# Kernel tuning notes

Measured on AMD Instinct MI355X. Metric: run time of the kernel, lower is better.

Reference implementation:

```python
import jax, jax.numpy as jnp
import numpy as np

MAX_H = 22
NUM_HEADS = 8
EPS = 1e-5
SLOPE = 0.01  # torch LeakyReLU default


def setup_inputs() -> dict:
    key = jax.random.key(0)
    ks = jax.random.split(key, 8)
    n, c, s, h, w = 16, 64, 30, 64, 22
    cp, v = 64, 17
    p, out_c = 7, 256
    D = c * MAX_H + cp * 2  # fuse_dim = 1536
    sil = jax.random.normal(ks[0], (n, c, s, h, w), dtype=jnp.float32)
    pose = jax.random.normal(ks[1], (n, cp, s, v), dtype=jnp.float32)
    min_idx = jax.random.randint(ks[2], (p, n), 0, h - MAX_H + 1, dtype=jnp.int32)
    max_idx = min_idx + MAX_H  # slices are exactly MAX_H rows (static shape)
    fc_bin = jax.random.normal(ks[3], (p, D, out_c), dtype=jnp.float32) * np.sqrt(2.0 / (D + out_c))
    gamma = 1.0 + 0.1 * jax.random.normal(ks[4], (out_c,), dtype=jnp.float32)
    beta = 0.1 * jax.random.normal(ks[5], (out_c,), dtype=jnp.float32)
    w_qkv = jax.random.normal(ks[6], (3 * out_c, out_c), dtype=jnp.float32) * 0.02
    w_proj = jax.random.normal(ks[7], (out_c, out_c), dtype=jnp.float32) * 0.02
    return {"sil": sil, "pose": pose, "fc_bin": fc_bin, "gamma": gamma, "beta": beta,
            "w_qkv": w_qkv, "w_proj": w_proj, "min_idx": min_idx, "max_idx": max_idx}


def _forward(sil, pose, fc_bin, gamma, beta, w_qkv, w_proj, min_idx):
    n, c, s, h, w = sil.shape
    p = min_idx.shape[0]
    sil_p = jnp.transpose(sil, (0, 2, 1, 3, 4))  # [n,s,c,h,w]
    parts = []
    for j in range(p):  # fixed small part loop; each gather is a big vectorized op
        idx = min_idx[j][:, None] + jnp.arange(MAX_H, dtype=min_idx.dtype)  # [n,MAX_H]
        g = jnp.take_along_axis(sil_p, idx[:, None, None, :, None], axis=3)  # [n,s,c,MAX_H,w]
        parts.append(g.mean(-1) + g.max(-1))  # mean + max pool over width
    silpart = jnp.stack(parts, 0)  # [p,n,s,c,MAX_H]
    silpart = jnp.transpose(silpart, (1, 2, 0, 3, 4)).reshape(n * s, p, c * MAX_H)

    cp, v = pose.shape[1], pose.shape[3]
    pose_r = jnp.transpose(pose, (0, 2, 1, 3)).reshape(n * s, cp, v)  # [ns,cp,17]
    # part 0: AdaptiveAvgPool1d(2) on 5 joints -> mean(j0..j2), mean(j2..j4)
    part0 = jnp.stack([pose_r[:, :, 0:3].mean(-1), pose_r[:, :, 2:5].mean(-1)], -1)  # [ns,cp,2]
    # parts 1..6: pairs of joints, pool(2->2) is identity
    others = pose_r[:, :, 5:].reshape(n * s, cp, 6, 2).transpose(0, 2, 1, 3)  # [ns,6,cp,2]
    posepart = jnp.concatenate([part0[:, None], others], axis=1)  # [ns,p,cp,2]
    posepart = jax.nn.leaky_relu(posepart, SLOPE).reshape(n * s, p, cp * 2)

    fuse = jnp.concatenate([silpart, posepart], axis=2)  # [ns,p,D]
    x = jnp.einsum('npd,pdo->npo', fuse, fc_bin)  # per-part FC -> [ns,p,out]

    # BatchNorm1d (training-mode batch stats) over [ns,out,p]
    x = jnp.transpose(x, (0, 2, 1))  # [ns,out,p]
    mu = x.mean((0, 2), keepdims=True)
    var = x.var((0, 2), keepdims=True)
    x = (x - mu) * jax.lax.rsqrt(var + EPS) * gamma[None, :, None] + beta[None, :, None]
    x = jnp.transpose(x, (0, 2, 1))  # [ns,p,out]

    # Attention over the p part tokens (note: source softmaxes over the HEAD axis)
    B, N, C = x.shape
    hd = C // NUM_HEADS
    qkv = (x @ w_qkv.T).reshape(B, N, 3, NUM_HEADS, hd).transpose(2, 0, 3, 1, 4)
    q, k, vv = qkv[0], qkv[1], qkv[2]  # [B,H,N,hd]
    attn = jnp.einsum('bhnd,bhmd->bhnm', q, k) * (hd ** -0.5)
    attn = jax.nn.softmax(attn, axis=1)  # faithful to attn.softmax(dim=1)
    ao = jnp.einsum('bhnm,bhmd->bhnd', attn, vv).transpose(0, 2, 1, 3).reshape(B, N, C)
    x = x + ao @ w_proj.T

    return x.reshape(n, s, p, C).transpose(0, 3, 1, 2)  # [n,out,s,p]


def reference(sil, pose, fc_bin, gamma, beta, w_qkv, w_proj, min_idx, max_idx):
    # max_idx == min_idx + MAX_H by construction; slice length is static MAX_H
    return _forward(sil, pose, fc_bin, gamma, beta, w_qkv, w_proj, min_idx)
```

## Files before the change

kernel.cpp:

```cpp
#include <hip/hip_runtime.h>
#include <hip/hip_bf16.h>
#include <math.h>

#define NS 480
#define NN 16
#define SS 30
#define CC 64
#define HHH 64
#define WW 22
#define PP 7
#define MAXH 22
#define CP 64
#define VV 17
#define DD 1536
#define OC 256
#define SILD 1408
#define NTOK 3360

typedef __bf16 bf16x8 __attribute__((ext_vector_type(8)));
typedef float f32x4 __attribute__((ext_vector_type(4)));
typedef short short8 __attribute__((ext_vector_type(8)));

__device__ __forceinline__ void gl_lds16(const void* g, void* l) {
    __builtin_amdgcn_global_load_lds(
        (const __attribute__((address_space(1))) void*)g,
        (__attribute__((address_space(3))) void*)l, 16, 0, 0);
}

__device__ __forceinline__ float bf2f(short s) {
    union { float f; unsigned u; } uu; uu.u = ((unsigned)(unsigned short)s) << 16; return uu.f;
}

__global__ __launch_bounds__(256) void rowfuse(const float* __restrict__ sil,
                                               const int* __restrict__ min_idx,
                                               __hip_bfloat16* __restrict__ fuse) {
    __shared__ float lds[256 * WW];
    __shared__ float hbuf[4][64];
    __shared__ int mi_s[112];
    int tid = threadIdx.x;
    if (tid < 112) mi_s[tid] = min_idx[tid];
    long long base = (long long)blockIdx.x * (256 * WW);
    const float4* src = (const float4*)(sil + base);
    float4* dst4 = (float4*)lds;
    for (int i = tid; i < 256 * WW / 4; i += 256) dst4[i] = src[i];
    __syncthreads();
    const float* row = lds + tid * WW;
    float s = 0.f, m = -INFINITY;
    #pragma unroll
    for (int k = 0; k < WW; k++) { float v = row[k]; s += v; m = fmaxf(m, v); }
    hbuf[tid >> 6][tid & 63] = s * (1.0f / WW) + m;
    __syncthreads();
    int q0 = blockIdx.x * 4;
    for (int idx = tid; idx < 4 * PP * MAXH; idx += 256) {
        int qi = idx / (PP * MAXH), r = idx % (PP * MAXH);
        int j = r / MAXH, hh = r % MAXH;
        int q = q0 + qi;
        int s_i = q % SS, t = q / SS;
        int c = t & 63, n = t >> 6;
        int mi = mi_s[j * NN + n];
        float v = hbuf[qi][mi + hh];
        fuse[((long long)(j * NS + n * SS + s_i)) * DD + c * MAXH + hh] = __float2bfloat16(v);
    }
}

__global__ __launch_bounds__(256) void weightprep(const float* __restrict__ wqkv,
                                                  const float* __restrict__ wproj,
                                                  const float* __restrict__ fcbin,
                                                  const float* __restrict__ pose,
                                                  __hip_bfloat16* __restrict__ wqkv16,
                                                  __hip_bfloat16* __restrict__ wproj16,
                                                  __hip_bfloat16* __restrict__ fcbinT16,
                                                  __hip_bfloat16* __restrict__ fuse) {
    int b = blockIdx.x;
    if (b < 768) { int g = b * 256 + threadIdx.x; wqkv16[g] = __float2bfloat16(wqkv[g]); return; }
    if (b < 1024) { int g = (b - 768) * 256 + threadIdx.x; wproj16[g] = __float2bfloat16(wproj[g]); return; }
    if (b < 1696) {
        __shared__ float t[64][65];
        int bb = b - 1024;
        int p = bb / 96, r2 = bb % 96, dt = r2 / 4, ot = r2 % 4;
        const float* s = fcbin + ((long long)p * DD + dt * 64) * OC + ot * 64;
        for (int i = threadIdx.x; i < 64 * 64; i += 256) {
            int r = i >> 6, c = i & 63;
            t[r][c] = s[(long long)r * OC + c];
        }
        __syncthreads();
        __hip_bfloat16* d = fcbinT16 + ((long long)p * OC + ot * 64) * DD + dt * 64;
        for (int i = threadIdx.x; i < 64 * 64; i += 256) {
            int r = i >> 6, c = i & 63;
            d[(long long)r * DD + c] = __float2bfloat16(t[c][r]);
        }
        return;
    }
    int g = (b - 1696) * 256 + threadIdx.x;
    int dd = g & 127;
    int t2 = g >> 7;
    int nsi = t2 % NS;
    int j = t2 / NS;
    int n = nsi / SS, s_i = nsi % SS;
    int cpi = dd >> 1, par = dd & 1;
    const float* pr = pose + (((long long)n * CP + cpi) * SS + s_i) * VV;
    float v;
    if (j == 0) {
        v = (par == 0) ? (pr[0] + pr[1] + pr[2]) * (1.f / 3.f)
                       : (pr[2] + pr[3] + pr[4]) * (1.f / 3.f);
    } else {
        v = pr[5 + (j - 1) * 2 + par];
    }
    v = (v > 0.f) ? v : 0.01f * v;
    fuse[(long long)(j * NS + nsi) * DD + SILD + dd] = __float2bfloat16(v);
}

template<bool ABF16, int EPI>
__global__ __launch_bounds__(256) void gemm2(
    const void* __restrict__ Ain, const __hip_bfloat16* __restrict__ Bt,
    float* __restrict__ Cf, __hip_bfloat16* __restrict__ Cb,
    float* __restrict__ partial, const float* __restrict__ ssb,
    int M, int N, int K, int lda, int ldc,
    long long aBatch, long long bBatch, long long cBatch)
{
    const __hip_bfloat16* Ab = (const __hip_bfloat16*)Ain + (ABF16 ? (long long)blockIdx.z * aBatch : 0);
    const float* Af = (const float*)Ain;
    const __hip_bfloat16* Bq = Bt + (long long)blockIdx.z * bBatch;
    float* C = Cf ? (Cf + (long long)blockIdx.z * cBatch) : nullptr;

    __shared__ short As[2][4096];
    __shared__ short Bs[2][4096];
    __shared__ float red[4][2][16][2];
    __shared__ float ssl[512];

    int tid = threadIdx.x, lane = tid & 63, w = tid >> 6;
    int wm = w >> 1, wn = w & 1;
    int row0 = blockIdx.x * 64, col0 = blockIdx.y * 64;

    if (!ABF16) {
        for (int i = tid; i < 512; i += 256) ssl[i] = ssb[i];
        __syncthreads();
    }

    f32x4 acc[2][2] = {};
    int nt = K >> 6;

    auto stageB = [&](int buf, int k0) {
        int cc = lane & 7;
        #pragma unroll
        for (int i = 0; i < 2; i++) {
            int r = w * 16 + i * 8 + (lane >> 3);
            int gcol = col0 + r; if (gcol >= N) gcol = N - 1;
            const char* g = (const char*)Bq + (((long long)gcol * K + k0) << 1) + ((cc ^ (r & 7)) << 4);
            gl_lds16(g, (char*)&Bs[buf][0] + (w * 16 + i * 8) * 128);
        }
    };
    auto stageA = [&](int buf, int k0) {
        if constexpr (ABF16) {
            int cc = lane & 7;
            #pragma unroll
            for (int i = 0; i < 2; i++) {
                int r = w * 16 + i * 8 + (lane >> 3);
                int grow = row0 + r; if (grow >= M) grow = M - 1;
                const char* g = (const char*)Ab + (((long long)grow * lda + k0) << 1) + ((cc ^ (r & 7)) << 4);
                gl_lds16(g, (char*)&As[buf][0] + (w * 16 + i * 8) * 128);
            }
        } else {
            #pragma unroll
            for (int i = 0; i < 2; i++) {
                int id = tid + i * 256;
                int r = id >> 3, c8 = id & 7;
                int grow = row0 + r; if (grow >= M) grow = M - 1;
                const float* src = Af + (long long)grow * lda + k0 + c8 * 8;
                float4 v0 = *(const float4*)src;
                float4 v1 = *(const float4*)(src + 4);
                int kb = k0 + c8 * 8;
                float vv[8] = {v0.x, v0.y, v0.z, v0.w, v1.x, v1.y, v1.z, v1.w};
                short8 o;
                #pragma unroll
                for (int j = 0; j < 8; j++) {
                    float tv = vv[j] * ssl[kb + j] + ssl[256 + kb + j];
                    union { __hip_bfloat16 h; short s; } u; u.h = __float2bfloat16(tv);
                    o[j] = u.s;
                }
                *(short8*)((char*)&As[buf][0] + r * 128 + ((c8 ^ (r & 7)) << 4)) = o;
            }
        }
    };

    stageA(0, 0); stageB(0, 0);
    __syncthreads();
    for (int t = 0; t < nt; t++) {
        int cur = t & 1;
        if (t + 1 < nt) { stageA(cur ^ 1, (t + 1) << 6); stageB(cur ^ 1, (t + 1) << 6); }
        #pragma unroll
        for (int ks = 0; ks < 2; ks++) {
            bf16x8 af[2], bfv[2];
            #pragma unroll
            for (int f = 0; f < 2; f++) {
                int r = wm * 32 + f * 16 + (lane & 15);
                int ca = (ks * 4 + (lane >> 4)) ^ (r & 7);
                af[f] = *(const bf16x8*)((const char*)&As[cur][0] + r * 128 + (ca << 4));
                int rb = wn * 32 + f * 16 + (lane & 15);
                int cb = (ks * 4 + (lane >> 4)) ^ (rb & 7);
                bfv[f] = *(const bf16x8*)((const char*)&Bs[cur][0] + rb * 128 + (cb << 4));
            }
            #pragma unroll
            for (int fm = 0; fm < 2; fm++)
                #pragma unroll
                for (int fn = 0; fn < 2; fn++)
                    acc[fm][fn] = __builtin_amdgcn_mfma_f32_16x16x32_bf16(
                        af[fm], bfv[fn], acc[fm][fn], 0, 0, 0);
        }
        __syncthreads();
    }

    if constexpr (EPI == 0) {
        float s[2] = {0.f, 0.f}, s2[2] = {0.f, 0.f};
        #pragma unroll
        for (int fm = 0; fm < 2; fm++) {
            #pragma unroll
            for (int fn = 0; fn < 2; fn++) {
                #pragma unroll
                for (int r4 = 0; r4 < 4; r4++) {
                    int grow = row0 + wm * 32 + fm * 16 + (lane >> 4) * 4 + r4;
                    int gcol = col0 + wn * 32 + fn * 16 + (lane & 15);
                    if (grow < M) {
                        float v = acc[fm][fn][r4];
                        C[(long long)grow * ldc + gcol] = v;
                        s[fn] += v; s2[fn] += v * v;
                    }
                }
            }
        }
        #pragma unroll
        for (int off = 16; off < 64; off <<= 1) {
            s[0] += __shfl_xor(s[0], off);  s2[0] += __shfl_xor(s2[0], off);
            s[1] += __shfl_xor(s[1], off);  s2[1] += __shfl_xor(s2[1], off);
        }
        if (lane < 16) {
            red[w][0][lane][0] = s[0]; red[w][0][lane][1] = s2[0];
            red[w][1][lane][0] = s[1]; red[w][1][lane][1] = s2[1];
        }
        __syncthreads();
        if (tid < 128) {
            int col = tid >> 1, which = tid & 1;
            int wn2 = (col >> 5) & 1, fn2 = (col >> 4) & 1, c16 = col & 15;
            float v = red[wn2][fn2][c16][which] + red[2 + wn2][fn2][c16][which];
            partial[((long long)(blockIdx.z * 8 + blockIdx.x) * 2 + which) * 256 + blockIdx.y * 64 + col] = v;
        }
    } else {
        #pragma unroll
        for (int fm = 0; fm < 2; fm++)
            #pragma unroll
            for (int fn = 0; fn < 2; fn++)
                #pragma unroll
                for (int r4 = 0; r4 < 4; r4++) {
                    int grow = row0 + wm * 32 + fm * 16 + (lane >> 4) * 4 + r4;
                    int gcol = col0 + wn * 32 + fn * 16 + (lane & 15);
                    if (grow < M) Cb[(long long)grow * ldc + gcol] = __float2bfloat16(acc[fm][fn][r4]);
                }
    }
}

__global__ __launch_bounds__(256) void bnfinal(const float* __restrict__ partial,
                                               const float* __restrict__ gamma,
                                               const float* __restrict__ beta,
                                               float* __restrict__ ssbuf) {
    int t = threadIdx.x;
    float s = 0.f, s2 = 0.f;
    for (int b = 0; b < 56; b++) { s += partial[b * 512 + t]; s2 += partial[b * 512 + 256 + t]; }
    float mu = s / (float)NTOK;
    float var = s2 / (float)NTOK - mu * mu;
    float rsig = rsqrtf(var + 1e-5f);
    float sc = gamma[t] * rsig;
    ssbuf[t] = sc;
    ssbuf[256 + t] = beta[t] - mu * sc;
}

__global__ __launch_bounds__(256) void attnproj(const __hip_bfloat16* __restrict__ qkv16,
                                                const __hip_bfloat16* __restrict__ wproj16,
                                                const float* __restrict__ xraw,
                                                const float* __restrict__ ssb,
                                                float* __restrict__ outp) {
    __shared__ float qs[14 * 768];
    __shared__ float as_[2][8][49];
    __shared__ short ao_s[16 * 256];
    __shared__ float Ct[256 * 17];
    __shared__ float ssl[512];

    int tid = threadIdx.x, lane = tid & 63, w = tid >> 6;
    int token0 = blockIdx.x * 14;

    for (int i = tid; i < 512; i += 256) ssl[i] = ssb[i];

    const short* src = (const short*)qkv16 + (long long)token0 * 768;
    for (int i = tid; i < 14 * 768 / 8; i += 256) {
        short8 v = *(const short8*)(src + i * 8);
        #pragma unroll
        for (int j = 0; j < 8; j++) qs[i * 8 + j] = bf2f(v[j]);
    }
    __syncthreads();
    for (int t = tid; t < 784; t += 256) {
        int bb = t / 392, r = t % 392, h = r / 49, ij = r % 49, i = ij / 7, j = ij % 7;
        const float* qp = qs + (bb * 7 + i) * 768 + h * 32;
        const float* kp = qs + (bb * 7 + j) * 768 + 256 + h * 32;
        float acc = 0.f;
        #pragma unroll
        for (int d = 0; d < 32; d++) acc += qp[d] * kp[d];
        as_[bb][h][ij] = acc * 0.17677669529663689f;
    }
    __syncthreads();
    if (tid < 98) {
        int bb = tid / 49, ij = tid % 49;
        float m = -INFINITY;
        #pragma unroll
        for (int h = 0; h < 8; h++) m = fmaxf(m, as_[bb][h][ij]);
        float e[8], sum = 0.f;
        #pragma unroll
        for (int h = 0; h < 8; h++) { e[h] = __expf(as_[bb][h][ij] - m); sum += e[h]; }
        float inv = 1.f / sum;
        #pragma unroll
        for (int h = 0; h < 8; h++) as_[bb][h][ij] = e[h] * inv;
    }
    __syncthreads();
    for (int t = tid; t < 16 * 256; t += 256) {
        int tl = t >> 8, col = t & 255;
        float acc = 0.f;
        if (tl < 14) {
            int bb = tl / 7, i = tl % 7, h = col >> 5;
            const float* ap = &as_[bb][h][i * 7];
            const float* vp = qs + (bb * 7) * 768 + 512 + col;
            #pragma unroll
            for (int j = 0; j < 7; j++) acc += ap[j] * vp[j * 768];
        }
        int c16 = col >> 3;
        union { __hip_bfloat16 h2; short s2; } u; u.h2 = __float2bfloat16(acc);
        ao_s[tl * 256 + ((c16 ^ (tl & 7)) << 3) + (col & 7)] = u.s2;
    }
    __syncthreads();
    f32x4 pacc[4] = {};
    int n0 = w * 64;
    #pragma unroll
    for (int k0 = 0; k0 < 256; k0 += 32) {
        int rowa = lane & 15;
        int kk = k0 + (lane >> 4) * 8;
        int c16a = kk >> 3;
        bf16x8 af = *(const bf16x8*)(const void*)&ao_s[rowa * 256 + ((c16a ^ (rowa & 7)) << 3)];
        #pragma unroll
        for (int fn = 0; fn < 4; fn++) {
            int n = n0 + fn * 16 + (lane & 15);
            bf16x8 bfv = *(const bf16x8*)(const void*)((const short*)wproj16 + n * 256 + kk);
            pacc[fn] = __builtin_amdgcn_mfma_f32_16x16x32_bf16(af, bfv, pacc[fn], 0, 0, 0);
        }
    }
    #pragma unroll
    for (int fn = 0; fn < 4; fn++)
        #pragma unroll
        for (int r4 = 0; r4 < 4; r4++) {
            int o = n0 + fn * 16 + (lane & 15);
            int t = (lane >> 4) * 4 + r4;
            Ct[o * 17 + t] = pacc[fn][r4];
        }
    __syncthreads();
    int o = tid;
    int n = token0 / 210, rem0 = token0 % 210;
    float* op = outp + ((long long)(n * 256 + o)) * 210 + rem0;
    float sc = ssl[o], sh = ssl[256 + o];
    #pragma unroll
    for (int t2 = 0; t2 < 14; t2 += 2) {
        float2 v;
        v.x = Ct[o * 17 + t2]     + xraw[(long long)(token0 + t2) * 256 + o] * sc + sh;
        v.y = Ct[o * 17 + t2 + 1] + xraw[(long long)(token0 + t2 + 1) * 256 + o] * sc + sh;
        *(float2*)(op + t2) = v;
    }
}

extern "C" void kernel_launch(void* const* d_in, const int* in_sizes, int n_in,
                              void* d_out, int out_size, void* d_ws, size_t ws_size,
                              hipStream_t stream) {
    const float* sil   = (const float*)d_in[0];
    const float* pose  = (const float*)d_in[1];
    const float* fcbin = (const float*)d_in[2];
    const float* gamma = (const float*)d_in[3];
    const float* beta  = (const float*)d_in[4];
    const float* wqkv  = (const float*)d_in[5];
    const float* wproj = (const float*)d_in[6];
    const int*   minidx= (const int*)d_in[7];
    float* out = (float*)d_out;

    float* ws = (float*)d_ws;
    __hip_bfloat16* fuse16   = (__hip_bfloat16*)ws;
    float* xraw    = ws + 2580480;
    float* partial = ws + 3440640;
    float* ssbuf   = ws + 3469312;
    __hip_bfloat16* wqkv16   = (__hip_bfloat16*)(ws + 3469824);
    __hip_bfloat16* wproj16  = (__hip_bfloat16*)(ws + 3568128);
    __hip_bfloat16* fcbinT16 = (__hip_bfloat16*)(ws + 3600896);
    __hip_bfloat16* qkv16    = (__hip_bfloat16*)(ws + 4977152);

    rowfuse<<<7680, 256, 0, stream>>>(sil, minidx, fuse16);
    weightprep<<<3376, 256, 0, stream>>>(wqkv, wproj, fcbin, pose,
                                         wqkv16, wproj16, fcbinT16, fuse16);
    gemm2<true, 0><<<dim3(8, 4, 7), 256, 0, stream>>>(fuse16, fcbinT16, xraw, nullptr,
        partial, nullptr,
        480, 256, 1536, 1536, 1792, (long long)480 * 1536, (long long)256 * 1536, 256);
    bnfinal<<<1, 256, 0, stream>>>(partial, gamma, beta, ssbuf);
    gemm2<false, 1><<<dim3(53, 12, 1), 256, 0, stream>>>(xraw, wqkv16, nullptr, qkv16,
        nullptr, ssbuf,
        3360, 768, 256, 256, 768, 0, 0, 0);
    attnproj<<<240, 256, 0, stream>>>(qkv16, wproj16, xraw, ssbuf, out);
}
```

Before: 83.31 us.

## Fuse prep kernels, fold BN stats and QKV GEMM into attention kernel

Merges the row pooling and weight/pose prep into one launch, and removes the separate BN-finalize and QKV GEMM launches. Each attention block now recomputes the BN scale/shift from the partial sums, normalizes its 14 tokens, and runs the QKV projection with MFMA in shared memory before attention. This drops two launches and the bf16 QKV round trip through global memory. In exchange, every block redundantly reduces the partials and streams the whole QKV weight matrix from global/L2, and the per-block work grows.

```diff
diff --git a/kernel.cpp b/kernel.cpp
--- a/kernel.cpp
+++ b/kernel.cpp
@@ -27,71 +27,68 @@
         (__attribute__((address_space(3))) void*)l, 16, 0, 0);
 }
 
-__device__ __forceinline__ float bf2f(short s) {
-    union { float f; unsigned u; } uu; uu.u = ((unsigned)(unsigned short)s) << 16; return uu.f;
-}
-
-__global__ __launch_bounds__(256) void rowfuse(const float* __restrict__ sil,
-                                               const int* __restrict__ min_idx,
-                                               __hip_bfloat16* __restrict__ fuse) {
-    __shared__ float lds[256 * WW];
-    __shared__ float hbuf[4][64];
-    __shared__ int mi_s[112];
-    int tid = threadIdx.x;
-    if (tid < 112) mi_s[tid] = min_idx[tid];
-    long long base = (long long)blockIdx.x * (256 * WW);
-    const float4* src = (const float4*)(sil + base);
-    float4* dst4 = (float4*)lds;
-    for (int i = tid; i < 256 * WW / 4; i += 256) dst4[i] = src[i];
-    __syncthreads();
-    const float* row = lds + tid * WW;
-    float s = 0.f, m = -INFINITY;
-    #pragma unroll
-    for (int k = 0; k < WW; k++) { float v = row[k]; s += v; m = fmaxf(m, v); }
-    hbuf[tid >> 6][tid & 63] = s * (1.0f / WW) + m;
-    __syncthreads();
-    int q0 = blockIdx.x * 4;
-    for (int idx = tid; idx < 4 * PP * MAXH; idx += 256) {
-        int qi = idx / (PP * MAXH), r = idx % (PP * MAXH);
-        int j = r / MAXH, hh = r % MAXH;
-        int q = q0 + qi;
-        int s_i = q % SS, t = q / SS;
-        int c = t & 63, n = t >> 6;
-        int mi = mi_s[j * NN + n];
-        float v = hbuf[qi][mi + hh];
-        fuse[((long long)(j * NS + n * SS + s_i)) * DD + c * MAXH + hh] = __float2bfloat16(v);
-    }
-}
-
-__global__ __launch_bounds__(256) void weightprep(const float* __restrict__ wqkv,
-                                                  const float* __restrict__ wproj,
-                                                  const float* __restrict__ fcbin,
-                                                  const float* __restrict__ pose,
-                                                  __hip_bfloat16* __restrict__ wqkv16,
-                                                  __hip_bfloat16* __restrict__ wproj16,
-                                                  __hip_bfloat16* __restrict__ fcbinT16,
-                                                  __hip_bfloat16* __restrict__ fuse) {
-    int b = blockIdx.x;
-    if (b < 768) { int g = b * 256 + threadIdx.x; wqkv16[g] = __float2bfloat16(wqkv[g]); return; }
-    if (b < 1024) { int g = (b - 768) * 256 + threadIdx.x; wproj16[g] = __float2bfloat16(wproj[g]); return; }
+__global__ __launch_bounds__(256) void prep(const float* __restrict__ sil,
+                                            const int* __restrict__ min_idx,
+                                            const float* __restrict__ wqkv,
+                                            const float* __restrict__ wproj,
+                                            const float* __restrict__ fcbin,
+                                            const float* __restrict__ pose,
+                                            __hip_bfloat16* __restrict__ fuse,
+                                            __hip_bfloat16* __restrict__ wqkv16,
+                                            __hip_bfloat16* __restrict__ wproj16,
+                                            __hip_bfloat16* __restrict__ fcbinT16) {
+    __shared__ __align__(16) char smem[24064];
+    int b = blockIdx.x, tid = threadIdx.x;
+    if (b < 7680) {
+        float* lds  = (float*)smem;
+        float* hbuf = (float*)(smem + 22528);
+        int*   mi_s = (int*)(smem + 23552);
+        if (tid < 112) mi_s[tid] = min_idx[tid];
+        long long base = (long long)b * (256 * WW);
+        const float4* src = (const float4*)(sil + base);
+        float4* dst4 = (float4*)lds;
+        for (int i = tid; i < 256 * WW / 4; i += 256) dst4[i] = src[i];
+        __syncthreads();
+        const float* row = lds + tid * WW;
+        float s = 0.f, m = -INFINITY;
+        #pragma unroll
+        for (int k = 0; k < WW; k++) { float v = row[k]; s += v; m = fmaxf(m, v); }
+        hbuf[tid] = s * (1.0f / WW) + m;
+        __syncthreads();
+        int q0 = b * 4;
+        for (int idx = tid; idx < 4 * PP * MAXH; idx += 256) {
+            int qi = idx / (PP * MAXH), r = idx % (PP * MAXH);
+            int j = r / MAXH, hh = r % MAXH;
+            int q = q0 + qi;
+            int s_i = q % SS, t = q / SS;
+            int c = t & 63, n = t >> 6;
+            int mi = mi_s[j * NN + n];
+            float v = hbuf[qi * 64 + mi + hh];
+            fuse[((long long)(j * NS + n * SS + s_i)) * DD + c * MAXH + hh] = __float2bfloat16(v);
+        }
+        return;
+    }
+    b -= 7680;
+    if (b < 768)  { int g = b * 256 + tid; wqkv16[g] = __float2bfloat16(wqkv[g]); return; }
+    if (b < 1024) { int g = (b - 768) * 256 + tid; wproj16[g] = __float2bfloat16(wproj[g]); return; }
     if (b < 1696) {
-        __shared__ float t[64][65];
+        float (*t)[65] = (float(*)[65])smem;
         int bb = b - 1024;
         int p = bb / 96, r2 = bb % 96, dt = r2 / 4, ot = r2 % 4;
         const float* s = fcbin + ((long long)p * DD + dt * 64) * OC + ot * 64;
-        for (int i = threadIdx.x; i < 64 * 64; i += 256) {
+        for (int i = tid; i < 64 * 64; i += 256) {
             int r = i >> 6, c = i & 63;
             t[r][c] = s[(long long)r * OC + c];
         }
         __syncthreads();
         __hip_bfloat16* d = fcbinT16 + ((long long)p * OC + ot * 64) * DD + dt * 64;
-        for (int i = threadIdx.x; i < 64 * 64; i += 256) {
+        for (int i = tid; i < 64 * 64; i += 256) {
             int r = i >> 6, c = i & 63;
             d[(long long)r * DD + c] = __float2bfloat16(t[c][r]);
         }
         return;
     }
-    int g = (b - 1696) * 256 + threadIdx.x;
+    int g = (b - 1696) * 256 + tid;
     int dd = g & 127;
     int t2 = g >> 7;
     int nsi = t2 % NS;
@@ -110,84 +107,44 @@
     fuse[(long long)(j * NS + nsi) * DD + SILD + dd] = __float2bfloat16(v);
 }
 
-template<bool ABF16, int EPI>
-__global__ __launch_bounds__(256) void gemm2(
-    const void* __restrict__ Ain, const __hip_bfloat16* __restrict__ Bt,
-    float* __restrict__ Cf, __hip_bfloat16* __restrict__ Cb,
-    float* __restrict__ partial, const float* __restrict__ ssb,
-    int M, int N, int K, int lda, int ldc,
-    long long aBatch, long long bBatch, long long cBatch)
+__global__ __launch_bounds__(256) void gemm_fc(
+    const __hip_bfloat16* __restrict__ Ain, const __hip_bfloat16* __restrict__ Bt,
+    float* __restrict__ Cf, float* __restrict__ partial)
 {
-    const __hip_bfloat16* Ab = (const __hip_bfloat16*)Ain + (ABF16 ? (long long)blockIdx.z * aBatch : 0);
-    const float* Af = (const float*)Ain;
-    const __hip_bfloat16* Bq = Bt + (long long)blockIdx.z * bBatch;
-    float* C = Cf ? (Cf + (long long)blockIdx.z * cBatch) : nullptr;
+    const int M = 480, N = 256, K = 1536, lda = 1536, ldc = 1792;
+    const __hip_bfloat16* Ab = Ain + (long long)blockIdx.z * 480 * 1536;
+    const __hip_bfloat16* Bq = Bt + (long long)blockIdx.z * 256 * 1536;
+    float* C = Cf + (long long)blockIdx.z * 256;
 
     __shared__ short As[2][4096];
     __shared__ short Bs[2][4096];
     __shared__ float red[4][2][16][2];
-    __shared__ float ssl[512];
 
     int tid = threadIdx.x, lane = tid & 63, w = tid >> 6;
     int wm = w >> 1, wn = w & 1;
     int row0 = blockIdx.x * 64, col0 = blockIdx.y * 64;
 
-    if (!ABF16) {
-        for (int i = tid; i < 512; i += 256) ssl[i] = ssb[i];
-        __syncthreads();
-    }
-
     f32x4 acc[2][2] = {};
     int nt = K >> 6;
 
-    auto stageB = [&](int buf, int k0) {
+    auto stage = [&](int buf, int k0) {
         int cc = lane & 7;
         #pragma unroll
         for (int i = 0; i < 2; i++) {
             int r = w * 16 + i * 8 + (lane >> 3);
-            int gcol = col0 + r; if (gcol >= N) gcol = N - 1;
-            const char* g = (const char*)Bq + (((long long)gcol * K + k0) << 1) + ((cc ^ (r & 7)) << 4);
-            gl_lds16(g, (char*)&Bs[buf][0] + (w * 16 + i * 8) * 128);
+            int grow = row0 + r; if (grow >= M) grow = M - 1;
+            const char* ga = (const char*)Ab + (((long long)grow * lda + k0) << 1) + ((cc ^ (r & 7)) << 4);
+            gl_lds16(ga, (char*)&As[buf][0] + (w * 16 + i * 8) * 128);
+            const char* gb = (const char*)Bq + (((long long)(col0 + r) * K + k0) << 1) + ((cc ^ (r & 7)) << 4);
+            gl_lds16(gb, (char*)&Bs[buf][0] + (w * 16 + i * 8) * 128);
         }
     };
-    auto stageA = [&](int buf, int k0) {
-        if constexpr (ABF16) {
-            int cc = lane & 7;
-            #pragma unroll
-            for (int i = 0; i < 2; i++) {
-                int r = w * 16 + i * 8 + (lane >> 3);
-                int grow = row0 + r; if (grow >= M) grow = M - 1;
-                const char* g = (const char*)Ab + (((long long)grow * lda + k0) << 1) + ((cc ^ (r & 7)) << 4);
-                gl_lds16(g, (char*)&As[buf][0] + (w * 16 + i * 8) * 128);
-            }
-        } else {
-            #pragma unroll
-            for (int i = 0; i < 2; i++) {
-                int id = tid + i * 256;
-                int r = id >> 3, c8 = id & 7;
-                int grow = row0 + r; if (grow >= M) grow = M - 1;
-                const float* src = Af + (long long)grow * lda + k0 + c8 * 8;
-                float4 v0 = *(const float4*)src;
-                float4 v1 = *(const float4*)(src + 4);
-                int kb = k0 + c8 * 8;
-                float vv[8] = {v0.x, v0.y, v0.z, v0.w, v1.x, v1.y, v1.z, v1.w};
-                short8 o;
-                #pragma unroll
-                for (int j = 0; j < 8; j++) {
-                    float tv = vv[j] * ssl[kb + j] + ssl[256 + kb + j];
-                    union { __hip_bfloat16 h; short s; } u; u.h = __float2bfloat16(tv);
-                    o[j] = u.s;
-                }
-                *(short8*)((char*)&As[buf][0] + r * 128 + ((c8 ^ (r & 7)) << 4)) = o;
-            }
-        }
-    };
-
-    stageA(0, 0); stageB(0, 0);
+
+    stage(0, 0);
     __syncthreads();
     for (int t = 0; t < nt; t++) {
         int cur = t & 1;
-        if (t + 1 < nt) { stageA(cur ^ 1, (t + 1) << 6); stageB(cur ^ 1, (t + 1) << 6); }
+        if (t + 1 < nt) stage(cur ^ 1, (t + 1) << 6);
         #pragma unroll
         for (int ks = 0; ks < 2; ks++) {
             bf16x8 af[2], bfv[2];
@@ -210,75 +167,54 @@
         __syncthreads();
     }
 
-    if constexpr (EPI == 0) {
-        float s[2] = {0.f, 0.f}, s2[2] = {0.f, 0.f};
-        #pragma unroll
-        for (int fm = 0; fm < 2; fm++) {
-            #pragma unroll
-            for (int fn = 0; fn < 2; fn++) {
-                #pragma unroll
-                for (int r4 = 0; r4 < 4; r4++) {
-                    int grow = row0 + wm * 32 + fm * 16 + (lane >> 4) * 4 + r4;
-                    int gcol = col0 + wn * 32 + fn * 16 + (lane & 15);
-                    if (grow < M) {
-                        float v = acc[fm][fn][r4];
-                        C[(long long)grow * ldc + gcol] = v;
-                        s[fn] += v; s2[fn] += v * v;
-                    }
+    float s[2] = {0.f, 0.f}, s2[2] = {0.f, 0.f};
+    #pragma unroll
+    for (int fm = 0; fm < 2; fm++) {
+        #pragma unroll
+        for (int fn = 0; fn < 2; fn++) {
+            #pragma unroll
+            for (int r4 = 0; r4 < 4; r4++) {
+                int grow = row0 + wm * 32 + fm * 16 + (lane >> 4) * 4 + r4;
+                int gcol = col0 + wn * 32 + fn * 16 + (lane & 15);
+                if (grow < M) {
+                    float v = acc[fm][fn][r4];
+                    C[(long long)grow * ldc + gcol] = v;
+                    s[fn] += v; s2[fn] += v * v;
                 }
             }
         }
-        #pragma unroll
-        for (int off = 16; off < 64; off <<= 1) {
-            s[0] += __shfl_xor(s[0], off);  s2[0] += __shfl_xor(s2[0], off);
-            s[1] += __shfl_xor(s[1], off);  s2[1] += __shfl_xor(s2[1], off);
-        }
-        if (lane < 16) {
-            red[w][0][lane][0] = s[0]; red[w][0][lane][1] = s2[0];
-            red[w][1][lane][0] = s[1]; red[w][1][lane][1] = s2[1];
-        }
-        __syncthreads();
-        if (tid < 128) {
-            int col = tid >> 1, which = tid & 1;
-            int wn2 = (col >> 5) & 1, fn2 = (col >> 4) & 1, c16 = col & 15;
-            float v = red[wn2][fn2][c16][which] + red[2 + wn2][fn2][c16][which];
-            partial[((long long)(blockIdx.z * 8 + blockIdx.x) * 2 + which) * 256 + blockIdx.y * 64 + col] = v;
-        }
-    } else {
-        #pragma unroll
-        for (int fm = 0; fm < 2; fm++)
-            #pragma unroll
-            for (int fn = 0; fn < 2; fn++)
-                #pragma unroll
-                for (int r4 = 0; r4 < 4; r4++) {
-                    int grow = row0 + wm * 32 + fm * 16 + (lane >> 4) * 4 + r4;
-                    int gcol = col0 + wn * 32 + fn * 16 + (lane & 15);
-                    if (grow < M) Cb[(long long)grow * ldc + gcol] = __float2bfloat16(acc[fm][fn][r4]);
-                }
-    }
-}
-
-__global__ __launch_bounds__(256) void bnfinal(const float* __restrict__ partial,
+    }
+    #pragma unroll
+    for (int off = 16; off < 64; off <<= 1) {
+        s[0] += __shfl_xor(s[0], off);  s2[0] += __shfl_xor(s2[0], off);
+        s[1] += __shfl_xor(s[1], off);  s2[1] += __shfl_xor(s2[1], off);
+    }
+    if (lane < 16) {
+        red[w][0][lane][0] = s[0]; red[w][0][lane][1] = s2[0];
+        red[w][1][lane][0] = s[1]; red[w][1][lane][1] = s2[1];
+    }
+    __syncthreads();
+    if (tid < 128) {
+        int col = tid >> 1, which = tid & 1;
+        int wn2 = (col >> 5) & 1, fn2 = (col >> 4) & 1, c16 = col & 15;
+        float v = red[wn2][fn2][c16][which] + red[2 + wn2][fn2][c16][which];
+        partial[((long long)(blockIdx.z * 8 + blockIdx.x) * 2 + which) * 256 + blockIdx.y * 64 + col] = v;
+    }
+}
+
+__device__ __forceinline__ float bf2f(short s) {
+    union { float f; unsigned u; } uu; uu.u = ((unsigned)(unsigned short)s) << 16; return uu.f;
+}
+
+__global__ __launch_bounds__(256) void qkvattn(const float* __restrict__ xraw,
+                                               const __hip_bfloat16* __restrict__ wqkv16,
+                                               const __hip_bfloat16* __restrict__ wproj16,
+                                               const float* __restrict__ partial,
                                                const float* __restrict__ gamma,
                                                const float* __restrict__ beta,
-                                               float* __restrict__ ssbuf) {
-    int t = threadIdx.x;
-    float s = 0.f, s2 = 0.f;
-    for (int b = 0; b < 56; b++) { s += partial[b * 512 + t]; s2 += partial[b * 512 + 256 + t]; }
-    float mu = s / (float)NTOK;
-    float var = s2 / (float)NTOK - mu * mu;
-    float rsig = rsqrtf(var + 1e-5f);
-    float sc = gamma[t] * rsig;
-    ssbuf[t] = sc;
-    ssbuf[256 + t] = beta[t] - mu * sc;
-}
-
-__global__ __launch_bounds__(256) void attnproj(const __hip_bfloat16* __restrict__ qkv16,
-                                                const __hip_bfloat16* __restrict__ wproj16,
-                                                const float* __restrict__ xraw,
-                                                const float* __restrict__ ssb,
-                                                float* __restrict__ outp) {
-    __shared__ float qs[14 * 768];
+                                               float* __restrict__ outp) {
+    __shared__ short As[16 * 256];
+    __shared__ float qkvs[14 * 768];
     __shared__ float as_[2][8][49];
     __shared__ short ao_s[16 * 256];
     __shared__ float Ct[256 * 17];
@@ -287,19 +223,71 @@
     int tid = threadIdx.x, lane = tid & 63, w = tid >> 6;
     int token0 = blockIdx.x * 14;
 
-    for (int i = tid; i < 512; i += 256) ssl[i] = ssb[i];
-
-    const short* src = (const short*)qkv16 + (long long)token0 * 768;
-    for (int i = tid; i < 14 * 768 / 8; i += 256) {
-        short8 v = *(const short8*)(src + i * 8);
-        #pragma unroll
-        for (int j = 0; j < 8; j++) qs[i * 8 + j] = bf2f(v[j]);
-    }
-    __syncthreads();
+    {
+        float s = 0.f, s2 = 0.f;
+        #pragma unroll 8
+        for (int bb = 0; bb < 56; bb++) {
+            s  += partial[bb * 512 + tid];
+            s2 += partial[bb * 512 + 256 + tid];
+        }
+        float mu = s * (1.f / NTOK);
+        float var = s2 * (1.f / NTOK) - mu * mu;
+        float rsig = rsqrtf(var + 1e-5f);
+        float sc = gamma[tid] * rsig;
+        ssl[tid] = sc;
+        ssl[256 + tid] = beta[tid] - mu * sc;
+    }
+    __syncthreads();
+
+    for (int i = tid; i < 512; i += 256) {
+        int r = i >> 5, c8 = i & 31;
+        short8 o = {};
+        if (r < 14) {
+            const float* src = xraw + (long long)(token0 + r) * 256 + c8 * 8;
+            float4 v0 = *(const float4*)src;
+            float4 v1 = *(const float4*)(src + 4);
+            float vv[8] = {v0.x, v0.y, v0.z, v0.w, v1.x, v1.y, v1.z, v1.w};
+            #pragma unroll
+            for (int j2 = 0; j2 < 8; j2++) {
+                float tv = vv[j2] * ssl[c8 * 8 + j2] + ssl[256 + c8 * 8 + j2];
+                union { __hip_bfloat16 h; short s; } u; u.h = __float2bfloat16(tv);
+                o[j2] = u.s;
+            }
+        }
+        *(short8*)&As[r * 256 + ((c8 ^ (r & 7)) << 3)] = o;
+    }
+    __syncthreads();
+
+    {
+        f32x4 qacc[12] = {};
+        int n0w = w * 192;
+        #pragma unroll
+        for (int k0 = 0; k0 < 256; k0 += 32) {
+            int r = lane & 15;
+            int kk = k0 + (lane >> 4) * 8;
+            int ck = kk >> 3;
+            bf16x8 af = *(const bf16x8*)(const void*)&As[r * 256 + ((ck ^ (r & 7)) << 3)];
+            #pragma unroll
+            for (int fn = 0; fn < 12; fn++) {
+                int nn2 = n0w + fn * 16 + (lane & 15);
+                bf16x8 bv = *(const bf16x8*)(const void*)((const short*)wqkv16 + nn2 * 256 + kk);
+                qacc[fn] = __builtin_amdgcn_mfma_f32_16x16x32_bf16(af, bv, qacc[fn], 0, 0, 0);
+            }
+        }
+        #pragma unroll
+        for (int fn = 0; fn < 12; fn++)
+            #pragma unroll
+            for (int r4 = 0; r4 < 4; r4++) {
+                int row = (lane >> 4) * 4 + r4;
+                if (row < 14) qkvs[row * 768 + n0w + fn * 16 + (lane & 15)] = qacc[fn][r4];
+            }
+    }
+    __syncthreads();
+
     for (int t = tid; t < 784; t += 256) {
         int bb = t / 392, r = t % 392, h = r / 49, ij = r % 49, i = ij / 7, j = ij % 7;
-        const float* qp = qs + (bb * 7 + i) * 768 + h * 32;
-        const float* kp = qs + (bb * 7 + j) * 768 + 256 + h * 32;
+        const float* qp = qkvs + (bb * 7 + i) * 768 + h * 32;
+        const float* kp = qkvs + (bb * 7 + j) * 768 + 256 + h * 32;
         float acc = 0.f;
         #pragma unroll
         for (int d = 0; d < 32; d++) acc += qp[d] * kp[d];
@@ -325,7 +313,7 @@
         if (tl < 14) {
             int bb = tl / 7, i = tl % 7, h = col >> 5;
             const float* ap = &as_[bb][h][i * 7];
-            const float* vp = qs + (bb * 7) * 768 + 512 + col;
+            const float* vp = qkvs + (bb * 7) * 768 + 512 + col;
             #pragma unroll
             for (int j = 0; j < 7; j++) acc += ap[j] * vp[j * 768];
         }
@@ -388,21 +376,12 @@
     __hip_bfloat16* fuse16   = (__hip_bfloat16*)ws;
     float* xraw    = ws + 2580480;
     float* partial = ws + 3440640;
-    float* ssbuf   = ws + 3469312;
-    __hip_bfloat16* wqkv16   = (__hip_bfloat16*)(ws + 3469824);
-    __hip_bfloat16* wproj16  = (__hip_bfloat16*)(ws + 3568128);
-    __hip_bfloat16* fcbinT16 = (__hip_bfloat16*)(ws + 3600896);
-    __hip_bfloat16* qkv16    = (__hip_bfloat16*)(ws + 4977152);
-
-    rowfuse<<<7680, 256, 0, stream>>>(sil, minidx, fuse16);
-    weightprep<<<3376, 256, 0, stream>>>(wqkv, wproj, fcbin, pose,
-                                         wqkv16, wproj16, fcbinT16, fuse16);
-    gemm2<true, 0><<<dim3(8, 4, 7), 256, 0, stream>>>(fuse16, fcbinT16, xraw, nullptr,
-        partial, nullptr,
-        480, 256, 1536, 1536, 1792, (long long)480 * 1536, (long long)256 * 1536, 256);
-    bnfinal<<<1, 256, 0, stream>>>(partial, gamma, beta, ssbuf);
-    gemm2<false, 1><<<dim3(53, 12, 1), 256, 0, stream>>>(xraw, wqkv16, nullptr, qkv16,
-        nullptr, ssbuf,
-        3360, 768, 256, 256, 768, 0, 0, 0);
-    attnproj<<<240, 256, 0, stream>>>(qkv16, wproj16, xraw, ssbuf, out);
-}
+    __hip_bfloat16* wqkv16   = (__hip_bfloat16*)(ws + 3469312);
+    __hip_bfloat16* wproj16  = (__hip_bfloat16*)(ws + 3567616);
+    __hip_bfloat16* fcbinT16 = (__hip_bfloat16*)(ws + 3600384);
+
+    prep<<<11056, 256, 0, stream>>>(sil, minidx, wqkv, wproj, fcbin, pose,
+                                    fuse16, wqkv16, wproj16, fcbinT16);
+    gemm_fc<<<dim3(8, 4, 7), 256, 0, stream>>>(fuse16, fcbinT16, xraw, partial);
+    qkvattn<<<240, 256, 0, stream>>>(xraw, wqkv16, wproj16, partial, gamma, beta, out);
+}
```

Result: no change. 83.53 us (+0.3%).
